# Performance work log

Hardware: AMD Instinct MI355X
Metric: run time of the kernel (lower is better)

Reference implementation:

```python
import jax, jax.numpy as jnp
import numpy as np

H = 8  # num_heads
NEG = -1e6  # mask fill value used by the torch masked_softmax


def layernorm(x, g, b, eps=1e-5):
    mu = jnp.mean(x, axis=-1, keepdims=True)
    var = jnp.mean(jnp.square(x - mu), axis=-1, keepdims=True)
    return (x - mu) * jax.lax.rsqrt(var + eps) * g + b


def setup_inputs() -> dict:
    key = jax.random.key(0)
    ks = jax.random.split(key, 10)
    B, S, D, F = 8, 1024, 512, 2048
    s = 0.02
    return {
        "X": jax.random.normal(ks[0], (B, S, D), jnp.float32),
        "valid_lens": jax.random.randint(ks[1], (B,), 1, S + 1, jnp.int32),
        "ln1_g": jnp.ones((D,), jnp.float32),
        "ln1_b": jnp.zeros((D,), jnp.float32),
        "Wq": jax.random.normal(ks[2], (D, D), jnp.float32) * s,
        "Wk": jax.random.normal(ks[3], (D, D), jnp.float32) * s,
        "Wv": jax.random.normal(ks[4], (D, D), jnp.float32) * s,
        "Wo": jax.random.normal(ks[5], (D, D), jnp.float32) * s,
        "ln2_g": jnp.ones((D,), jnp.float32),
        "ln2_b": jnp.zeros((D,), jnp.float32),
        "W1": jax.random.normal(ks[6], (D, F), jnp.float32) * s,
        "b1": jnp.zeros((F,), jnp.float32),
        "W2": jax.random.normal(ks[7], (F, D), jnp.float32) * s,
        "b2": jnp.zeros((D,), jnp.float32),
    }


def vit_block(X, valid_lens, ln1_g, ln1_b, Wq, Wk, Wv, Wo, ln2_g, ln2_b, W1, b1, W2, b2):
    B, S, D = X.shape
    dh = D // H
    h = layernorm(X, ln1_g, ln1_b)
    # project and split heads: [B, S, H, dh]
    q = (h @ Wq).reshape(B, S, H, dh)
    k = (h @ Wk).reshape(B, S, H, dh)
    v = (h @ Wv).reshape(B, S, H, dh)
    scores = jnp.einsum("bqhd,bkhd->bhqk", q, k) / jnp.sqrt(jnp.float32(dh))
    # mask keys >= valid_len[b] with -1e6 (as in masked_softmax)
    mask = jnp.arange(S)[None, None, None, :] < valid_lens[:, None, None, None]
    scores = jnp.where(mask, scores, NEG)
    attn = jax.nn.softmax(scores, axis=-1)
    out = jnp.einsum("bhqk,bkhd->bqhd", attn, v).reshape(B, S, D)
    X = X + out @ Wo
    h2 = layernorm(X, ln2_g, ln2_b)
    mlp = jax.nn.gelu(h2 @ W1 + b1, approximate=False) @ W2 + b2
    return X + mlp


def reference(X, valid_lens, ln1_g, ln1_b, Wq, Wk, Wv, Wo, ln2_g, ln2_b, W1, b1, W2, b2):
    return vit_block(X, valid_lens, ln1_g, ln1_b, Wq, Wk, Wv, Wo, ln2_g, ln2_b, W1, b1, W2, b2)
```

## Files before the change

### kernel.cpp

```cpp
#include <hip/hip_runtime.h>
#include <math.h>

#define BB 8
#define SS 1024
#define DD 512
#define FF 2048
#define NH 8
#define MM (BB * SS)
#define LDQKV 1536

using bf8 = __attribute__((ext_vector_type(8))) short;
using f4  = __attribute__((ext_vector_type(4))) float;

#define AS1 __attribute__((address_space(1)))
#define AS3 __attribute__((address_space(3)))

__device__ __forceinline__ void gload16(const void* g, void* l) {
  __builtin_amdgcn_global_load_lds((AS1 const void*)g, (AS3 void*)l, 16, 0, 0);
}

template <int N> __device__ __forceinline__ void wait_vm() {
  if constexpr (N == 0)      asm volatile("s_waitcnt vmcnt(0)" ::: "memory");
  else if constexpr (N == 3) asm volatile("s_waitcnt vmcnt(3)" ::: "memory");
  else if constexpr (N == 4) asm volatile("s_waitcnt vmcnt(4)" ::: "memory");
  else                       asm volatile("s_waitcnt vmcnt(8)" ::: "memory");
  __builtin_amdgcn_sched_barrier(0);
}

__device__ __forceinline__ void bar() {
  __builtin_amdgcn_sched_barrier(0);
  __builtin_amdgcn_s_barrier();
  __builtin_amdgcn_sched_barrier(0);
}

__device__ __forceinline__ void lgk0() {
  asm volatile("s_waitcnt lgkmcnt(0)" ::: "memory");
  __builtin_amdgcn_sched_barrier(0);
}

__device__ __forceinline__ unsigned short f2b(float f) {
  union { float f; unsigned u; } v; v.f = f;
  unsigned r = v.u + 0x7fffu + ((v.u >> 16) & 1u);
  return (unsigned short)(r >> 16);
}

__device__ __forceinline__ float gelu_f(float x) {
  float ax = fabsf(x) * 0.70710678118654752f;
  float t = 1.0f / (1.0f + 0.3275911f * ax);
  float poly = t * (0.254829592f +
               t * (-0.284496736f +
               t * (1.421413741f +
               t * (-1.453152027f + t * 1.061405429f))));
  float erfv = 1.0f - poly * __expf(-ax * ax);
  erfv = copysignf(erfv, x);
  return 0.5f * x * (1.0f + erfv);
}

__global__ __launch_bounds__(256) void ln_bf16(const float* __restrict__ x,
                                               const float* __restrict__ g,
                                               const float* __restrict__ bta,
                                               unsigned short* __restrict__ out) {
  int wave = threadIdx.x >> 6, lane = threadIdx.x & 63;
  int row = (blockIdx.x << 2) + wave;
  const float* xr = x + (size_t)row * DD;
  int base = lane << 3;
  float4 v0 = *(const float4*)(xr + base);
  float4 v1 = *(const float4*)(xr + base + 4);
  float s  = v0.x + v0.y + v0.z + v0.w + v1.x + v1.y + v1.z + v1.w;
  float sq = v0.x*v0.x + v0.y*v0.y + v0.z*v0.z + v0.w*v0.w
           + v1.x*v1.x + v1.y*v1.y + v1.z*v1.z + v1.w*v1.w;
  for (int m = 32; m; m >>= 1) { s += __shfl_xor(s, m); sq += __shfl_xor(sq, m); }
  float mu  = s * (1.0f / DD);
  float var = sq * (1.0f / DD) - mu * mu;
  float rs  = rsqrtf(var + 1e-5f);
  float xv[8], go[8], bo[8];
  *(float4*)(xv) = v0; *(float4*)(xv + 4) = v1;
  *(float4*)(go)     = *(const float4*)(g + base);
  *(float4*)(go + 4) = *(const float4*)(g + base + 4);
  *(float4*)(bo)     = *(const float4*)(bta + base);
  *(float4*)(bo + 4) = *(const float4*)(bta + base + 4);
  union { unsigned short u[8]; uint4 v; } ov;
#pragma unroll
  for (int i = 0; i < 8; i++) ov.u[i] = f2b((xv[i] - mu) * rs * go[i] + bo[i]);
  *(uint4*)(out + (size_t)row * DD + base) = ov.v;
}

__global__ __launch_bounds__(256) void tconv(const float* __restrict__ in,
                                             unsigned short* __restrict__ outp,
                                             int K, int N) {
  __shared__ float tile[32][33];
  int n0 = blockIdx.x << 5, k0 = blockIdx.y << 5;
  int c = threadIdx.x & 31, r = threadIdx.x >> 5;
#pragma unroll
  for (int i = 0; i < 4; i++)
    tile[r + 8 * i][c] = in[(size_t)(k0 + r + 8 * i) * N + n0 + c];
  __syncthreads();
#pragma unroll
  for (int i = 0; i < 4; i++)
    outp[(size_t)(n0 + r + 8 * i) * K + k0 + c] = f2b(tile[c][r + 8 * i]);
}

__global__ __launch_bounds__(256) void tconv4(
    const float* __restrict__ s0, const float* __restrict__ s1,
    const float* __restrict__ s2, const float* __restrict__ s3,
    unsigned short* __restrict__ d0, unsigned short* __restrict__ d1,
    unsigned short* __restrict__ d2, unsigned short* __restrict__ d3) {
  __shared__ float tile[32][33];
  const float* in; unsigned short* outp;
  switch (blockIdx.z) {
    case 0: in = s0; outp = d0; break;
    case 1: in = s1; outp = d1; break;
    case 2: in = s2; outp = d2; break;
    default: in = s3; outp = d3; break;
  }
  int n0 = blockIdx.x << 5, k0 = blockIdx.y << 5;
  int c = threadIdx.x & 31, r = threadIdx.x >> 5;
#pragma unroll
  for (int i = 0; i < 4; i++)
    tile[r + 8 * i][c] = in[(size_t)(k0 + r + 8 * i) * DD + n0 + c];
  __syncthreads();
#pragma unroll
  for (int i = 0; i < 4; i++)
    outp[(size_t)(n0 + r + 8 * i) * DD + k0 + c] = f2b(tile[c][r + 8 * i]);
}

#define MQ256(g, g2)                                                         \
  do {                                                                       \
    __builtin_amdgcn_s_setprio(1);                                           \
    _Pragma("unroll") for (int mi = 0; mi < 4; mi++)                         \
      _Pragma("unroll") for (int u = 0; u < 2; u++)                          \
        _Pragma("unroll") for (int k2 = 0; k2 < 2; k2++)                     \
          acc[(g) * 4 + mi][(g2) * 2 + u] =                                  \
              __builtin_amdgcn_mfma_f32_16x16x32_bf16(                       \
                  af[mi][k2], bfr[(g2) * 2 + u][k2],                         \
                  acc[(g) * 4 + mi][(g2) * 2 + u], 0, 0, 0);                 \
    __builtin_amdgcn_s_setprio(0);                                           \
  } while (0)

#define LB256(g2, buf)                                                       \
  do {                                                                       \
    _Pragma("unroll") for (int u = 0; u < 2; u++) {                          \
      int r = rb + ((g2) * 2 + u) * 16 + r4;                                 \
      _Pragma("unroll") for (int k2 = 0; k2 < 2; k2++)                       \
        bfr[(g2) * 2 + u][k2] = *(const bf8*)((const char*)Bs[buf][hb] +     \
            r * 128 + ((((k2 << 2) | ksl) ^ (r & 7)) << 4));                 \
    }                                                                        \
  } while (0)

template <int ACT>
__global__ __launch_bounds__(512, 1) void gemm256(
    const unsigned short* __restrict__ A,
    const unsigned short* __restrict__ Bt,
    const float* __restrict__ bias,
    unsigned short* __restrict__ Cb,
    int M, int N, int K, int gx) {
  __shared__ unsigned short As[2][2][128 * 64];
  __shared__ unsigned short Bs[2][2][128 * 64];
  int tid = threadIdx.x, wid = tid >> 6, lane = tid & 63;

  int bid = blockIdx.x, cpx = (int)gridDim.x >> 3;
  int swz = (bid & 7) * cpx + (bid >> 3);
  int m0 = (swz / gx) << 8, n0 = (swz % gx) << 8;

  int wm = (wid >> 2) << 7;
  int wn = (wid & 3) << 6;
  int ha = wm >> 7, hb = wn >> 7, rb = wn & 64;
  int r4 = lane & 15, ksl = lane >> 4;
  int srow = lane >> 3, gs = (lane & 7) ^ srow;

  f4 acc[8][4];
#pragma unroll
  for (int i = 0; i < 8; i++)
#pragma unroll
    for (int j = 0; j < 4; j++) acc[i][j] = (f4){0.f, 0.f, 0.f, 0.f};
  bf8 af[4][2], bfr[4][2];

  auto SA = [&](int h, int t) {
    int buf = t & 1, k0 = t << 6;
#pragma unroll
    for (int i = 0; i < 2; i++) {
      int ch = wid * 2 + i;
      gload16(A + (size_t)(m0 + h * 128 + ch * 8 + srow) * K + k0 + gs * 8,
              &As[buf][h][ch * 512]);
    }
  };
  auto SB = [&](int h, int t) {
    int buf = t & 1, k0 = t << 6;
#pragma unroll
    for (int i = 0; i < 2; i++) {
      int ch = wid * 2 + i;
      gload16(Bt + (size_t)(n0 + h * 128 + ch * 8 + srow) * K + k0 + gs * 8,
              &Bs[buf][h][ch * 512]);
    }
  };
  auto LA = [&](int g, int buf) {
#pragma unroll
    for (int mi = 0; mi < 4; mi++) {
      int r = g * 64 + mi * 16 + r4;
#pragma unroll
      for (int k2 = 0; k2 < 2; k2++)
        af[mi][k2] = *(const bf8*)((const char*)As[buf][ha] + r * 128 +
                                   ((((k2 << 2) | ksl) ^ (r & 7)) << 4));
    }
  };

  int nt = K >> 6;
  SB(0, 0); SB(1, 0); SA(0, 0); SA(1, 0); SB(0, 1); SB(1, 1);
  wait_vm<4>();
  bar();

  for (int T = 0; T < nt; T++) {
    int buf = T & 1;
    LA(0, buf);
    LB256(0, buf);
    if (T + 1 < nt) SA(0, T + 1);
    bar(); lgk0();
    MQ256(0, 0);
    bar();
    LB256(1, buf);
    if (T + 1 < nt) SA(1, T + 1);
    bar(); lgk0();
    MQ256(0, 1);
    bar();
    LA(1, buf);
    if (T + 2 < nt) SB(0, T + 2);
    bar(); lgk0();
    MQ256(1, 0);
    bar();
    if (T + 2 < nt) SB(1, T + 2);
    bar(); lgk0();
    MQ256(1, 1);
    if (T + 1 < nt) {
      if (T + 2 < nt) wait_vm<4>();
      else            wait_vm<0>();
    }
    bar();
  }
  wait_vm<0>();

  int rq = ksl << 2;
  float bv[4];
#pragma unroll
  for (int ni = 0; ni < 4; ni++)
    bv[ni] = bias ? bias[n0 + wn + ni * 16 + r4] : 0.0f;
#pragma unroll
  for (int mi = 0; mi < 8; mi++) {
#pragma unroll
    for (int j = 0; j < 4; j++) {
      int row = m0 + wm + mi * 16 + rq + j;
#pragma unroll
      for (int ni = 0; ni < 4; ni++) {
        int col = n0 + wn + ni * 16 + r4;
        float v = acc[mi][ni][j] + bv[ni];
        if (ACT) v = gelu_f(v);
        Cb[(size_t)row * N + col] = f2b(v);
      }
    }
  }
}

template <int BM, int BN, int ACT>
__global__ __launch_bounds__(256, 4) void gemm_t(
    const unsigned short* __restrict__ A,
    const unsigned short* __restrict__ Bt,
    const float* __restrict__ bias,
    const float* __restrict__ res,
    float* __restrict__ Cf,
    unsigned short* __restrict__ Cb,
    int M, int N, int K, int gx) {
  constexpr int WM = BM / 2, WN = BN / 2;
  constexpr int FM = WM / 16, FN = WN / 16;
  constexpr int NCHA = BM / 16;
  constexpr int NCH = (BM + BN) / 16;
  constexpr int L = NCH / 4;
  __shared__ unsigned short As[2][BM * 32];
  __shared__ unsigned short Bs[2][BN * 32];
  int tid = threadIdx.x, wid = tid >> 6, lane = tid & 63;

  int bid = blockIdx.x, cpx = (int)gridDim.x >> 3;
  int swz = (bid & 7) * cpx + (bid >> 3);
  int m0 = (swz / gx) * BM, n0 = (swz % gx) * BN;

  int wm = (wid >> 1) * WM, wn = (wid & 1) * WN;
  int r4 = lane & 15, ksl = lane >> 4;
  int srow = lane >> 2, gs = lane & 3;

  f4 acc[FM][FN];
#pragma unroll
  for (int i = 0; i < FM; i++)
#pragma unroll
    for (int j = 0; j < FN; j++) acc[i][j] = (f4){0.f, 0.f, 0.f, 0.f};

  auto STAGE = [&](int buf, int t) {
    int k0 = t << 5;
#pragma unroll
    for (int i = 0; i < L; i++) {
      int c = wid * L + i;
      if (c < NCHA)
        gload16(A + (size_t)(m0 + c * 16 + srow) * K + k0 + gs * 8,
                &As[buf][c * 512]);
      else
        gload16(Bt + (size_t)(n0 + (c - NCHA) * 16 + srow) * K + k0 + gs * 8,
                &Bs[buf][(c - NCHA) * 512]);
    }
  };

  auto COMPUTE = [&](int buf) {
    bf8 af[FM], bfr[FN];
#pragma unroll
    for (int mi = 0; mi < FM; mi++)
      af[mi] = *(const bf8*)((const char*)&As[buf][0] +
                             (wm + mi * 16 + r4) * 64 + ksl * 16);
#pragma unroll
    for (int ni = 0; ni < FN; ni++)
      bfr[ni] = *(const bf8*)((const char*)&Bs[buf][0] +
                              (wn + ni * 16 + r4) * 64 + ksl * 16);
    __builtin_amdgcn_s_setprio(1);
#pragma unroll
    for (int mi = 0; mi < FM; mi++)
#pragma unroll
      for (int ni = 0; ni < FN; ni++)
        acc[mi][ni] = __builtin_amdgcn_mfma_f32_16x16x32_bf16(
            af[mi], bfr[ni], acc[mi][ni], 0, 0, 0);
    __builtin_amdgcn_s_setprio(0);
  };

  int nt = K >> 5;
  STAGE(0, 0);
  STAGE(1, 1);
  for (int t = 0; t < nt; t++) {
    if (t + 1 < nt) wait_vm<L>();
    else            wait_vm<0>();
    bar();
    COMPUTE(t & 1);
    bar();
    if (t + 2 < nt) STAGE(t & 1, t + 2);
  }

  int rq = ksl << 2;
  float bv[FN];
#pragma unroll
  for (int ni = 0; ni < FN; ni++)
    bv[ni] = bias ? bias[n0 + wn + ni * 16 + r4] : 0.0f;
#pragma unroll
  for (int mi = 0; mi < FM; mi++) {
#pragma unroll
    for (int j = 0; j < 4; j++) {
      int row = m0 + wm + mi * 16 + rq + j;
#pragma unroll
      for (int ni = 0; ni < FN; ni++) {
        int col = n0 + wn + ni * 16 + r4;
        float v = acc[mi][ni][j] + bv[ni];
        if (ACT) v = gelu_f(v);
        if (res) v += res[(size_t)row * N + col];
        if (Cf) Cf[(size_t)row * N + col] = v;
        else    Cb[(size_t)row * N + col] = f2b(v);
      }
    }
  }
}

__global__ __launch_bounds__(256) void attn_mfma(
    const unsigned short* __restrict__ QKV,
    const int* __restrict__ vlen,
    unsigned short* __restrict__ AO) {
  __shared__ unsigned short Qs[64 * 64];
  __shared__ unsigned short Ks[64 * 64];
  __shared__ unsigned short Vt[64 * 64];
  __shared__ unsigned short Ps[64 * 64];
  int b = blockIdx.z, h = blockIdx.y, q0 = blockIdx.x << 6;
  int tid = threadIdx.x, wid = tid >> 6, lane = tid & 63;
  int vl = vlen[b];
  int r4 = lane & 15, ksl = lane >> 4;

  int srow = lane >> 3;
  int gs = (lane & 7) ^ srow;
  {
    const unsigned short* qsrc =
        QKV + (size_t)(b * SS + q0 + wid * 16 + srow) * LDQKV + h * 64 + gs * 8;
    gload16(qsrc, Qs + wid * 1024);
    gload16(qsrc + (size_t)8 * LDQKV, Qs + wid * 1024 + 512);
  }
  const unsigned short* kbase =
      QKV + (size_t)(b * SS + wid * 16 + srow) * LDQKV + DD + h * 64 + gs * 8;
  int vp = tid & 31, vdg = (tid >> 5) << 3;
  const unsigned short* vbase =
      QKV + (size_t)(b * SS + 2 * vp) * LDQKV + 2 * DD + h * 64 + vdg;

  f4 o[4];
#pragma unroll
  for (int i = 0; i < 4; i++) o[i] = (f4){0.f, 0.f, 0.f, 0.f};
  float mrun[4], lrun[4];
#pragma unroll
  for (int j = 0; j < 4; j++) { mrun[j] = -3e38f; lrun[j] = 0.0f; }

  int ntiles = (vl + 63) >> 6;
  if (ntiles > 16) ntiles = 16;

  for (int t = 0; t < ntiles; t++) {
    int kg0 = t << 6;
    const unsigned short* ks = kbase + (size_t)kg0 * LDQKV;
    gload16(ks, Ks + wid * 1024);
    gload16(ks + (size_t)8 * LDQKV, Ks + wid * 1024 + 512);
    {
      const unsigned short* v0 = vbase + (size_t)kg0 * LDQKV;
      const unsigned short* v1 = v0 + LDQKV;
      unsigned short va[8], vb[8];
      *(uint4*)va = *(const uint4*)v0;
      *(uint4*)vb = *(const uint4*)v1;
#pragma unroll
      for (int i = 0; i < 8; i++) {
        int d = vdg + i;
        unsigned val = (unsigned)va[i] | ((unsigned)vb[i] << 16);
        int byte = (d << 7) + (((vp >> 2) ^ (d & 7)) << 4) + ((vp & 3) << 2);
        *(unsigned*)((char*)Vt + byte) = val;
      }
    }
    __syncthreads();

    f4 s[4];
#pragma unroll
    for (int i = 0; i < 4; i++) s[i] = (f4){0.f, 0.f, 0.f, 0.f};
#pragma unroll
    for (int k2 = 0; k2 < 2; k2++) {
      int slot = (k2 << 2) + ksl;
      int qr = (wid << 4) + r4;
      bf8 aq = *(const bf8*)((const char*)Qs + (qr << 7) + ((slot ^ (qr & 7)) << 4));
#pragma unroll
      for (int ni = 0; ni < 4; ni++) {
        int kr = (ni << 4) + r4;
        bf8 bk = *(const bf8*)((const char*)Ks + (kr << 7) + ((slot ^ (kr & 7)) << 4));
        s[ni] = __builtin_amdgcn_mfma_f32_16x16x32_bf16(aq, bk, s[ni], 0, 0, 0);
      }
    }

#pragma unroll
    for (int j = 0; j < 4; j++) {
      int qr = (wid << 4) + ((lane >> 4) << 2) + j;
      float sv[4], mx = -3e38f;
#pragma unroll
      for (int ni = 0; ni < 4; ni++) {
        float v = s[ni][j] * 0.125f;
        if (kg0 + (ni << 4) + r4 >= vl) v = -1e6f;
        sv[ni] = v;
        mx = fmaxf(mx, v);
      }
#pragma unroll
      for (int m2 = 1; m2 < 16; m2 <<= 1) mx = fmaxf(mx, __shfl_xor(mx, m2));
      float mnew = fmaxf(mrun[j], mx);
      float al = __expf(mrun[j] - mnew);
      float ls = 0.0f;
      unsigned short pb[4];
#pragma unroll
      for (int ni = 0; ni < 4; ni++) {
        float p = __expf(sv[ni] - mnew);
        ls += p;
        pb[ni] = f2b(p);
      }
#pragma unroll
      for (int m2 = 1; m2 < 16; m2 <<= 1) ls += __shfl_xor(ls, m2);
      lrun[j] = lrun[j] * al + ls;
      mrun[j] = mnew;
#pragma unroll
      for (int ni = 0; ni < 4; ni++) {
        int kc = (ni << 4) + r4;
        int byte = (qr << 7) + (((kc >> 3) ^ (qr & 7)) << 4) + ((kc & 7) << 1);
        *(unsigned short*)((char*)Ps + byte) = pb[ni];
        o[ni][j] *= al;
      }
    }

#pragma unroll
    for (int k2 = 0; k2 < 2; k2++) {
      int slot = (k2 << 2) + ksl;
      int qr = (wid << 4) + r4;
      bf8 ap = *(const bf8*)((const char*)Ps + (qr << 7) + ((slot ^ (qr & 7)) << 4));
#pragma unroll
      for (int ni = 0; ni < 4; ni++) {
        int dr = (ni << 4) + r4;
        bf8 bv = *(const bf8*)((const char*)Vt + (dr << 7) + ((slot ^ (dr & 7)) << 4));
        o[ni] = __builtin_amdgcn_mfma_f32_16x16x32_bf16(ap, bv, o[ni], 0, 0, 0);
      }
    }
    __syncthreads();
  }

  float inv[4];
#pragma unroll
  for (int j = 0; j < 4; j++) inv[j] = 1.0f / lrun[j];
#pragma unroll
  for (int ni = 0; ni < 4; ni++) {
#pragma unroll
    for (int j = 0; j < 4; j++) {
      int qr = (wid << 4) + ((lane >> 4) << 2) + j;
      int d = (ni << 4) + r4;
      AO[(size_t)(b * SS + q0 + qr) * DD + h * 64 + d] = f2b(o[ni][j] * inv[j]);
    }
  }
}

extern "C" void kernel_launch(void* const* d_in, const int* in_sizes, int n_in,
                              void* d_out, int out_size, void* d_ws,
                              size_t ws_size, hipStream_t stream) {
  const float* X    = (const float*)d_in[0];
  const int*   vln  = (const int*)d_in[1];
  const float* ln1g = (const float*)d_in[2];
  const float* ln1b = (const float*)d_in[3];
  const float* Wq   = (const float*)d_in[4];
  const float* Wk   = (const float*)d_in[5];
  const float* Wv   = (const float*)d_in[6];
  const float* Wo   = (const float*)d_in[7];
  const float* ln2g = (const float*)d_in[8];
  const float* ln2b = (const float*)d_in[9];
  const float* W1   = (const float*)d_in[10];
  const float* b1   = (const float*)d_in[11];
  const float* W2   = (const float*)d_in[12];
  const float* b2   = (const float*)d_in[13];
  float* out = (float*)d_out;

  unsigned short* ws = (unsigned short*)d_ws;
  unsigned short* h     = ws;
  unsigned short* QKVb  = h     + (size_t)MM * DD;
  unsigned short* AOb   = QKVb  + (size_t)MM * LDQKV;
  unsigned short* mid   = AOb   + (size_t)MM * DD;
  unsigned short* Wqkvt = mid   + (size_t)MM * FF;
  unsigned short* Wot   = Wqkvt + (size_t)3 * DD * DD;
  unsigned short* W1t   = Wot   + (size_t)DD * DD;
  unsigned short* W2t   = W1t   + (size_t)FF * DD;

  dim3 blk(256);
  dim3 blk8(512);

  tconv4<<<dim3(16, 16, 4), blk, 0, stream>>>(
      Wq, Wk, Wv, Wo, Wqkvt, Wqkvt + (size_t)DD * DD,
      Wqkvt + (size_t)2 * DD * DD, Wot);
  tconv<<<dim3(64, 16), blk, 0, stream>>>(W1, W1t, DD, FF);
  tconv<<<dim3(16, 64), blk, 0, stream>>>(W2, W2t, FF, DD);

  ln_bf16<<<dim3(MM / 4), blk, 0, stream>>>(X, ln1g, ln1b, h);
  gemm256<0><<<dim3((LDQKV / 256) * (MM / 256)), blk8, 0, stream>>>(
      h, Wqkvt, nullptr, QKVb, MM, LDQKV, DD, LDQKV / 256);
  attn_mfma<<<dim3(SS / 64, NH, BB), blk, 0, stream>>>(QKVb, vln, AOb);
  gemm_t<128, 64, 0><<<dim3((DD / 64) * (MM / 128)), blk, 0, stream>>>(
      AOb, Wot, nullptr, X, out, nullptr, MM, DD, DD, DD / 64);
  ln_bf16<<<dim3(MM / 4), blk, 0, stream>>>(out, ln2g, ln2b, h);
  gemm256<1><<<dim3((FF / 256) * (MM / 256)), blk8, 0, stream>>>(
      h, W1t, b1, mid, MM, FF, DD, FF / 256);
  gemm_t<128, 64, 0><<<dim3((DD / 64) * (MM / 128)), blk, 0, stream>>>(
      mid, W2t, b2, out, out, nullptr, MM, DD, FF, DD / 64);
}
```

Before: 180.3 us.

## Replace 256x256 block GEMM with per-wave 64x64 tiles, swizzle gemm_t LDS

The QKV and W1 GEMMs move from a 512-thread 256x256 block tile with block-wide barriers to a 128-thread kernel where each wave independently computes its own 64x64 output tile. Each wave stages its own LDS slice and uses no barriers. The gemm_t LDS layout gains an XOR swizzle to avoid bank conflicts, its occupancy hint rises to 6, and epilogue loops are reordered column-outer. Much smaller tiles cut operand reuse and raise global and L2 traffic, in exchange for removing synchronisation and raising occupancy.

```diff
diff --git a/kernel.cpp b/kernel.cpp
--- a/kernel.cpp
+++ b/kernel.cpp
@@ -23,7 +23,8 @@
   if constexpr (N == 0)      asm volatile("s_waitcnt vmcnt(0)" ::: "memory");
   else if constexpr (N == 3) asm volatile("s_waitcnt vmcnt(3)" ::: "memory");
   else if constexpr (N == 4) asm volatile("s_waitcnt vmcnt(4)" ::: "memory");
-  else                       asm volatile("s_waitcnt vmcnt(8)" ::: "memory");
+  else if constexpr (N == 8) asm volatile("s_waitcnt vmcnt(8)" ::: "memory");
+  else                       asm volatile("s_waitcnt vmcnt(16)" ::: "memory");
   __builtin_amdgcn_sched_barrier(0);
 }
 
@@ -124,133 +125,93 @@
     outp[(size_t)(n0 + r + 8 * i) * DD + k0 + c] = f2b(tile[c][r + 8 * i]);
 }
 
-#define MQ256(g, g2)                                                         \
-  do {                                                                       \
-    __builtin_amdgcn_s_setprio(1);                                           \
-    _Pragma("unroll") for (int mi = 0; mi < 4; mi++)                         \
-      _Pragma("unroll") for (int u = 0; u < 2; u++)                          \
-        _Pragma("unroll") for (int k2 = 0; k2 < 2; k2++)                     \
-          acc[(g) * 4 + mi][(g2) * 2 + u] =                                  \
-              __builtin_amdgcn_mfma_f32_16x16x32_bf16(                       \
-                  af[mi][k2], bfr[(g2) * 2 + u][k2],                         \
-                  acc[(g) * 4 + mi][(g2) * 2 + u], 0, 0, 0);                 \
-    __builtin_amdgcn_s_setprio(0);                                           \
-  } while (0)
-
-#define LB256(g2, buf)                                                       \
-  do {                                                                       \
-    _Pragma("unroll") for (int u = 0; u < 2; u++) {                          \
-      int r = rb + ((g2) * 2 + u) * 16 + r4;                                 \
-      _Pragma("unroll") for (int k2 = 0; k2 < 2; k2++)                       \
-        bfr[(g2) * 2 + u][k2] = *(const bf8*)((const char*)Bs[buf][hb] +     \
-            r * 128 + ((((k2 << 2) | ksl) ^ (r & 7)) << 4));                 \
-    }                                                                        \
-  } while (0)
-
 template <int ACT>
-__global__ __launch_bounds__(512, 1) void gemm256(
+__global__ __launch_bounds__(128, 2) void gemm_wp(
     const unsigned short* __restrict__ A,
     const unsigned short* __restrict__ Bt,
     const float* __restrict__ bias,
     unsigned short* __restrict__ Cb,
-    int M, int N, int K, int gx) {
-  __shared__ unsigned short As[2][2][128 * 64];
-  __shared__ unsigned short Bs[2][2][128 * 64];
-  int tid = threadIdx.x, wid = tid >> 6, lane = tid & 63;
+    int M, int N, int K, int gxn) {
+  __shared__ unsigned short Lds[2][2][4096];
+  int tid = threadIdx.x, wv = tid >> 6, lane = tid & 63;
 
   int bid = blockIdx.x, cpx = (int)gridDim.x >> 3;
   int swz = (bid & 7) * cpx + (bid >> 3);
-  int m0 = (swz / gx) << 8, n0 = (swz % gx) << 8;
-
-  int wm = (wid >> 2) << 7;
-  int wn = (wid & 3) << 6;
-  int ha = wm >> 7, hb = wn >> 7, rb = wn & 64;
+  int tile = swz * 2 + wv;
+  int m0 = (tile / gxn) << 6, n0 = (tile % gxn) << 6;
+
   int r4 = lane & 15, ksl = lane >> 4;
-  int srow = lane >> 3, gs = (lane & 7) ^ srow;
-
-  f4 acc[8][4];
-#pragma unroll
-  for (int i = 0; i < 8; i++)
+  int srow = lane >> 2;
+  int gs = (lane & 3) ^ ((lane >> 3) & 3);
+
+  const unsigned short* aSrc = A + (size_t)(m0 + srow) * K + gs * 8;
+  const unsigned short* bSrc = Bt + (size_t)(n0 + srow) * K + gs * 8;
+  char* lw = (char*)&Lds[wv][0][0];
+
+  f4 acc[4][4];
+#pragma unroll
+  for (int i = 0; i < 4; i++)
 #pragma unroll
     for (int j = 0; j < 4; j++) acc[i][j] = (f4){0.f, 0.f, 0.f, 0.f};
-  bf8 af[4][2], bfr[4][2];
-
-  auto SA = [&](int h, int t) {
-    int buf = t & 1, k0 = t << 6;
-#pragma unroll
-    for (int i = 0; i < 2; i++) {
-      int ch = wid * 2 + i;
-      gload16(A + (size_t)(m0 + h * 128 + ch * 8 + srow) * K + k0 + gs * 8,
-              &As[buf][h][ch * 512]);
+
+  auto STAGE = [&](int buf, int t) {
+    int k0 = t << 5;
+#pragma unroll
+    for (int ch = 0; ch < 4; ch++) {
+      gload16(aSrc + (size_t)(ch * 16) * K + k0, &Lds[wv][buf][ch * 512]);
+      gload16(bSrc + (size_t)(ch * 16) * K + k0, &Lds[wv][buf][2048 + ch * 512]);
     }
   };
-  auto SB = [&](int h, int t) {
-    int buf = t & 1, k0 = t << 6;
-#pragma unroll
-    for (int i = 0; i < 2; i++) {
-      int ch = wid * 2 + i;
-      gload16(Bt + (size_t)(n0 + h * 128 + ch * 8 + srow) * K + k0 + gs * 8,
-              &Bs[buf][h][ch * 512]);
-    }
+
+  auto COMPUTE = [&](int buf) {
+    char* ab = lw + buf * 8192;
+    bf8 af[4], bfr[4];
+#pragma unroll
+    for (int mi = 0; mi < 4; mi++) {
+      int r = mi * 16 + r4;
+      af[mi] = *(const bf8*)(ab + r * 64 + ((ksl ^ ((r >> 1) & 3)) << 4));
+    }
+#pragma unroll
+    for (int ni = 0; ni < 4; ni++) {
+      int r = ni * 16 + r4;
+      bfr[ni] = *(const bf8*)(ab + 4096 + r * 64 + ((ksl ^ ((r >> 1) & 3)) << 4));
+    }
+    __builtin_amdgcn_s_setprio(1);
+#pragma unroll
+    for (int mi = 0; mi < 4; mi++)
+#pragma unroll
+      for (int ni = 0; ni < 4; ni++)
+        acc[mi][ni] = __builtin_amdgcn_mfma_f32_16x16x32_bf16(
+            af[mi], bfr[ni], acc[mi][ni], 0, 0, 0);
+    __builtin_amdgcn_s_setprio(0);
   };
-  auto LA = [&](int g, int buf) {
-#pragma unroll
-    for (int mi = 0; mi < 4; mi++) {
-      int r = g * 64 + mi * 16 + r4;
-#pragma unroll
-      for (int k2 = 0; k2 < 2; k2++)
-        af[mi][k2] = *(const bf8*)((const char*)As[buf][ha] + r * 128 +
-                                   ((((k2 << 2) | ksl) ^ (r & 7)) << 4));
-    }
-  };
-
-  int nt = K >> 6;
-  SB(0, 0); SB(1, 0); SA(0, 0); SA(1, 0); SB(0, 1); SB(1, 1);
-  wait_vm<4>();
-  bar();
-
-  for (int T = 0; T < nt; T++) {
-    int buf = T & 1;
-    LA(0, buf);
-    LB256(0, buf);
-    if (T + 1 < nt) SA(0, T + 1);
-    bar(); lgk0();
-    MQ256(0, 0);
-    bar();
-    LB256(1, buf);
-    if (T + 1 < nt) SA(1, T + 1);
-    bar(); lgk0();
-    MQ256(0, 1);
-    bar();
-    LA(1, buf);
-    if (T + 2 < nt) SB(0, T + 2);
-    bar(); lgk0();
-    MQ256(1, 0);
-    bar();
-    if (T + 2 < nt) SB(1, T + 2);
-    bar(); lgk0();
-    MQ256(1, 1);
-    if (T + 1 < nt) {
-      if (T + 2 < nt) wait_vm<4>();
-      else            wait_vm<0>();
-    }
-    bar();
-  }
-  wait_vm<0>();
+
+  int nt = K >> 5;
+  STAGE(0, 0);
+  STAGE(1, 1);
+  for (int t = 0; t < nt; t++) {
+    if (t + 1 < nt) wait_vm<8>();
+    else            wait_vm<0>();
+    COMPUTE(t & 1);
+    if (t + 2 < nt) {
+      lgk0();
+      STAGE(t & 1, t + 2);
+    }
+  }
 
   int rq = ksl << 2;
   float bv[4];
 #pragma unroll
   for (int ni = 0; ni < 4; ni++)
-    bv[ni] = bias ? bias[n0 + wn + ni * 16 + r4] : 0.0f;
-#pragma unroll
-  for (int mi = 0; mi < 8; mi++) {
-#pragma unroll
-    for (int j = 0; j < 4; j++) {
-      int row = m0 + wm + mi * 16 + rq + j;
-#pragma unroll
-      for (int ni = 0; ni < 4; ni++) {
-        int col = n0 + wn + ni * 16 + r4;
+    bv[ni] = bias ? bias[n0 + ni * 16 + r4] : 0.0f;
+#pragma unroll
+  for (int ni = 0; ni < 4; ni++) {
+    int col = n0 + ni * 16 + r4;
+#pragma unroll
+    for (int mi = 0; mi < 4; mi++) {
+#pragma unroll
+      for (int j = 0; j < 4; j++) {
+        int row = m0 + mi * 16 + rq + j;
         float v = acc[mi][ni][j] + bv[ni];
         if (ACT) v = gelu_f(v);
         Cb[(size_t)row * N + col] = f2b(v);
@@ -259,8 +220,8 @@
   }
 }
 
-template <int BM, int BN, int ACT>
-__global__ __launch_bounds__(256, 4) void gemm_t(
+template <int BM, int BN, int ACT, int MINW>
+__global__ __launch_bounds__(256, MINW) void gemm_t(
     const unsigned short* __restrict__ A,
     const unsigned short* __restrict__ Bt,
     const float* __restrict__ bias,
@@ -283,7 +244,7 @@
 
   int wm = (wid >> 1) * WM, wn = (wid & 1) * WN;
   int r4 = lane & 15, ksl = lane >> 4;
-  int srow = lane >> 2, gs = lane & 3;
+  int srow = lane >> 2, gs = (lane & 3) ^ ((lane >> 3) & 3);
 
   f4 acc[FM][FN];
 #pragma unroll
@@ -308,13 +269,17 @@
   auto COMPUTE = [&](int buf) {
     bf8 af[FM], bfr[FN];
 #pragma unroll
-    for (int mi = 0; mi < FM; mi++)
-      af[mi] = *(const bf8*)((const char*)&As[buf][0] +
-                             (wm + mi * 16 + r4) * 64 + ksl * 16);
-#pragma unroll
-    for (int ni = 0; ni < FN; ni++)
-      bfr[ni] = *(const bf8*)((const char*)&Bs[buf][0] +
-                              (wn + ni * 16 + r4) * 64 + ksl * 16);
+    for (int mi = 0; mi < FM; mi++) {
+      int r = wm + mi * 16 + r4;
+      af[mi] = *(const bf8*)((const char*)&As[buf][0] + r * 64 +
+                             ((ksl ^ ((r >> 1) & 3)) << 4));
+    }
+#pragma unroll
+    for (int ni = 0; ni < FN; ni++) {
+      int r = wn + ni * 16 + r4;
+      bfr[ni] = *(const bf8*)((const char*)&Bs[buf][0] + r * 64 +
+                              ((ksl ^ ((r >> 1) & 3)) << 4));
+    }
     __builtin_amdgcn_s_setprio(1);
 #pragma unroll
     for (int mi = 0; mi < FM; mi++)
@@ -343,13 +308,13 @@
   for (int ni = 0; ni < FN; ni++)
     bv[ni] = bias ? bias[n0 + wn + ni * 16 + r4] : 0.0f;
 #pragma unroll
-  for (int mi = 0; mi < FM; mi++) {
-#pragma unroll
-    for (int j = 0; j < 4; j++) {
-      int row = m0 + wm + mi * 16 + rq + j;
-#pragma unroll
-      for (int ni = 0; ni < FN; ni++) {
-        int col = n0 + wn + ni * 16 + r4;
+  for (int ni = 0; ni < FN; ni++) {
+    int col = n0 + wn + ni * 16 + r4;
+#pragma unroll
+    for (int mi = 0; mi < FM; mi++) {
+#pragma unroll
+      for (int j = 0; j < 4; j++) {
+        int row = m0 + wm + mi * 16 + rq + j;
         float v = acc[mi][ni][j] + bv[ni];
         if (ACT) v = gelu_f(v);
         if (res) v += res[(size_t)row * N + col];
@@ -529,7 +494,7 @@
   unsigned short* W2t   = W1t   + (size_t)FF * DD;
 
   dim3 blk(256);
-  dim3 blk8(512);
+  dim3 blkw(128);
 
   tconv4<<<dim3(16, 16, 4), blk, 0, stream>>>(
       Wq, Wk, Wv, Wo, Wqkvt, Wqkvt + (size_t)DD * DD,
@@ -538,14 +503,14 @@
   tconv<<<dim3(16, 64), blk, 0, stream>>>(W2, W2t, FF, DD);
 
   ln_bf16<<<dim3(MM / 4), blk, 0, stream>>>(X, ln1g, ln1b, h);
-  gemm256<0><<<dim3((LDQKV / 256) * (MM / 256)), blk8, 0, stream>>>(
-      h, Wqkvt, nullptr, QKVb, MM, LDQKV, DD, LDQKV / 256);
+  gemm_wp<0><<<dim3((MM / 64) * (LDQKV / 64) / 2), blkw, 0, stream>>>(
+      h, Wqkvt, nullptr, QKVb, MM, LDQKV, DD, LDQKV / 64);
   attn_mfma<<<dim3(SS / 64, NH, BB), blk, 0, stream>>>(QKVb, vln, AOb);
-  gemm_t<128, 64, 0><<<dim3((DD / 64) * (MM / 128)), blk, 0, stream>>>(
+  gemm_t<128, 64, 0, 6><<<dim3((DD / 64) * (MM / 128)), blk, 0, stream>>>(
       AOb, Wot, nullptr, X, out, nullptr, MM, DD, DD, DD / 64);
   ln_bf16<<<dim3(MM / 4), blk, 0, stream>>>(out, ln2g, ln2b, h);
-  gemm256<1><<<dim3((FF / 256) * (MM / 256)), blk8, 0, stream>>>(
-      h, W1t, b1, mid, MM, FF, DD, FF / 256);
-  gemm_t<128, 64, 0><<<dim3((DD / 64) * (MM / 128)), blk, 0, stream>>>(
+  gemm_wp<1><<<dim3((MM / 64) * (FF / 64) / 2), blkw, 0, stream>>>(
+      h, W1t, b1, mid, MM, FF, DD, FF / 64);
+  gemm_t<128, 64, 0, 6><<<dim3((DD / 64) * (MM / 128)), blk, 0, stream>>>(
       mid, W2t, b2, out, out, nullptr, MM, DD, FF, DD / 64);
 }
```

Measured after the change: 201.1 us. 1.12x slower.
